# Kernel optimization log

Measured on AMD Instinct MI355X. Metric: run time of the kernel, lower is better.

## Reference

```python
import jax, jax.numpy as jnp
import numpy as np

B, T, E, D, V, L, A = 32, 800, 512, 1024, 5000, 149, 512
SOS, EOS = 1, 2


def setup_inputs() -> dict:
    key = jax.random.key(0)
    ks = jax.random.split(key, 20)
    s = 0.02
    inp = {
        'hpad': jax.random.normal(ks[0], (B, T, E), dtype=jnp.float32),
        'hlen': jax.random.randint(ks[1], (B,), T // 2, T + 1),
        'ys': jax.random.randint(ks[2], (B, L), 3, V),
        # embedding + output projection
        'embed': jax.random.normal(ks[3], (V, D), dtype=jnp.float32) * s,
        'W_out': jax.random.normal(ks[4], (V, D), dtype=jnp.float32) * s,
        'b_out': jnp.zeros((V,), dtype=jnp.float32),
        # additive attention params
        'W_enc': jax.random.normal(ks[5], (E, A), dtype=jnp.float32) * s,
        'W_dec': jax.random.normal(ks[6], (D, A), dtype=jnp.float32) * s,
        'v_att': jax.random.normal(ks[7], (A,), dtype=jnp.float32) * s,
        # LSTMCell layer 0: input = [ey; att_c] of size D+E
        'W_ih0': jax.random.normal(ks[8], (4 * D, D + E), dtype=jnp.float32) * s,
        'b_ih0': jnp.zeros((4 * D,), dtype=jnp.float32),
        'W_hh0': jax.random.normal(ks[9], (4 * D, D), dtype=jnp.float32) * s,
        'b_hh0': jnp.zeros((4 * D,), dtype=jnp.float32),
        # LSTMCell layer 1: input = z0 of size D
        'W_ih1': jax.random.normal(ks[10], (4 * D, D), dtype=jnp.float32) * s,
        'b_ih1': jnp.zeros((4 * D,), dtype=jnp.float32),
        'W_hh1': jax.random.normal(ks[11], (4 * D, D), dtype=jnp.float32) * s,
        'b_hh1': jnp.zeros((4 * D,), dtype=jnp.float32),
    }
    return inp


def _lstm_cell(x, h, c, W_ih, b_ih, W_hh, b_hh):
    # torch.nn.LSTMCell gate order: i, f, g, o
    g = x @ W_ih.T + b_ih + h @ W_hh.T + b_hh
    i, f, gg, o = jnp.split(g, 4, axis=-1)
    c2 = jax.nn.sigmoid(f) * c + jax.nn.sigmoid(i) * jnp.tanh(gg)
    h2 = jax.nn.sigmoid(o) * jnp.tanh(c2)
    return h2, c2


def reference(hpad, hlen, ys, embed, W_out, b_out, W_enc, W_dec, v_att,
              W_ih0, b_ih0, W_hh0, b_hh0, W_ih1, b_ih1, W_hh1, b_hh1):
    mask = jnp.arange(T)[None, :] < hlen[:, None]          # [B,T]
    hpad = hpad * mask[..., None]                          # mask_by_length
    ys_in = jnp.concatenate([jnp.full((B, 1), SOS, ys.dtype), ys], axis=1)   # [B,L+1]
    ys_out = jnp.concatenate([ys, jnp.full((B, 1), EOS, ys.dtype)], axis=1)  # [B,L+1]
    eys = embed[ys_in]                                     # [B,L+1,D]
    pe = jnp.einsum('bte,ea->bta', hpad, W_enc)            # precomputed enc proj

    def step(carry, ey):
        z0, c0, z1, c1 = carry
        # additive attention: e = v^T tanh(W_enc h + W_dec z0)
        e = jnp.einsum('bta,a->bt', jnp.tanh(pe + (z0 @ W_dec)[:, None, :]), v_att)
        e = jnp.where(mask, e, -1e30)
        w = jax.nn.softmax(e, axis=-1)                     # [B,T]
        att_c = jnp.einsum('bt,bte->be', w, hpad)          # [B,E]
        z0, c0 = _lstm_cell(jnp.concatenate([ey, att_c], axis=1), z0, c0,
                            W_ih0, b_ih0, W_hh0, b_hh0)
        z1, c1 = _lstm_cell(z0, z1, c1, W_ih1, b_ih1, W_hh1, b_hh1)
        logits = z1 @ W_out.T + b_out                      # [B,V]
        return (z0, c0, z1, c1), logits

    z = jnp.zeros((B, D), dtype=hpad.dtype)
    carry0 = (z, z, z, z)
    _, logits = jax.lax.scan(step, carry0, eys.transpose(1, 0, 2))  # [L+1,B,V]
    logits = logits.transpose(1, 0, 2)                     # [B,L+1,V]

    logp = jax.nn.log_softmax(logits, axis=-1)
    nll = -jnp.take_along_axis(logp, ys_out[..., None], axis=-1)[..., 0]
    # F.cross_entropy mean, then * (mean(len ys_in) - 1) = * L
    loss = nll.mean() * L
    acc = (jnp.argmax(logits, axis=-1) == ys_out).mean()
    return loss, acc
```

## Files before the change

kernel.cpp:

```cpp
#include <hip/hip_runtime.h>


typedef unsigned short u16;
typedef unsigned char u8;
typedef long long i64;
typedef unsigned long long u64;
typedef float f32x4 __attribute__((ext_vector_type(4)));
typedef float f32x2 __attribute__((ext_vector_type(2)));
typedef short s16x8 __attribute__((ext_vector_type(8)));

constexpr int cB = 32, cT = 800, cE = 512, cD = 1024, cV = 5000, cL = 149,
              cNS = 150, cA = 512;
constexpr int SOS = 1, EOS = 2;
constexpr int NBLK = 256;
constexpr float DS = 1.0f / 128.0f;

__device__ __forceinline__ float bf2f(u16 x){
  union { unsigned u; float f; } v; v.u = ((unsigned)x) << 16; return v.f;
}
__device__ __forceinline__ u16 f2bf(float f){
  union { float f; unsigned u; } v; v.f = f;
  unsigned r = v.u + 0x7FFFu + ((v.u >> 16) & 1u);
  return (u16)(r >> 16);
}
__device__ __forceinline__ float frcp(float x){ return __builtin_amdgcn_rcpf(x); }
__device__ __forceinline__ float fsigm(float x){ return frcp(1.f + __expf(-x)); }
__device__ __forceinline__ float ftanh(float x){
  float u = __expf(2.f * x);
  return 1.f - 2.f * frcp(u + 1.f);
}
__device__ __forceinline__ f32x4 MFMA(s16x8 a, s16x8 b, f32x4 c){
  return __builtin_amdgcn_mfma_f32_16x16x32_bf16(a, b, c, 0, 0, 0);
}
__device__ __forceinline__ f32x4 MFMA8(i64 a, i64 b, f32x4 c){
  return __builtin_amdgcn_mfma_f32_16x16x32_fp8_fp8(a, b, c, 0, 0, 0);
}
__device__ __forceinline__ s16x8 LD8(const u16* p){ return *(const s16x8*)p; }
__device__ __forceinline__ u8 f2fp8(float x){
  return (u8)(__builtin_amdgcn_cvt_pk_fp8_f32(x, x, 0, false) & 0xFF);
}
__device__ __forceinline__ unsigned pk4(float a, float b, float c, float d){
  unsigned w = (unsigned)__builtin_amdgcn_cvt_pk_fp8_f32(a, b, 0, false);
  w = (unsigned)__builtin_amdgcn_cvt_pk_fp8_f32(c, d, (int)w, true);
  return w;
}
__device__ __forceinline__ void unpack8(unsigned lo, unsigned hi, float* o){
  f32x2 a = __builtin_amdgcn_cvt_pk_f32_fp8((int)lo, false);
  f32x2 b = __builtin_amdgcn_cvt_pk_f32_fp8((int)lo, true);
  f32x2 c = __builtin_amdgcn_cvt_pk_f32_fp8((int)hi, false);
  f32x2 d = __builtin_amdgcn_cvt_pk_f32_fp8((int)hi, true);
  o[0]=a[0]; o[1]=a[1]; o[2]=b[0]; o[3]=b[1];
  o[4]=c[0]; o[5]=c[1]; o[6]=d[0]; o[7]=d[1];
}

__device__ __forceinline__ float ld_sc(const float* p){
  return __hip_atomic_load(p, __ATOMIC_RELAXED, __HIP_MEMORY_SCOPE_AGENT);
}
__device__ __forceinline__ void st_sc(float* p, float v){
  __hip_atomic_store(p, v, __ATOMIC_RELAXED, __HIP_MEMORY_SCOPE_AGENT);
}
__device__ __forceinline__ u64 ld_sc8(const void* p){
  return __hip_atomic_load((const u64*)p, __ATOMIC_RELAXED, __HIP_MEMORY_SCOPE_AGENT);
}
__device__ __forceinline__ void st_scb(u8* p, u8 v){
  __hip_atomic_store(p, v, __ATOMIC_RELAXED, __HIP_MEMORY_SCOPE_AGENT);
}

__global__ void k_init(int* bar, float* q, float* c0, float* c1, u8* z1f8,
                       float* att_acc, float* att_l){
  int i = blockIdx.x * blockDim.x + threadIdx.x, n = gridDim.x * blockDim.x;
  for (int k = i; k < 512; k += n) bar[k] = 0;
  for (int k = i; k < cB * cA; k += n) q[k] = 0.f;
  for (int k = i; k < 2 * cB * cD; k += n){ c0[k] = 0.f; c1[k] = 0.f; }
  for (int k = i; k < cB * cD / 4; k += n) ((unsigned*)z1f8)[k] = 0;
  for (int k = i; k < cB * cE; k += n) att_acc[k] = 0.f;
  for (int k = i; k < cB; k += n) att_l[k] = 0.f;
}

__global__ void k_cvt(const float* __restrict__ s, u16* __restrict__ d, int n4){
  int i = blockIdx.x * blockDim.x + threadIdx.x, st = gridDim.x * blockDim.x;
  for (int k = i; k < n4; k += st){
    float4 v = ((const float4*)s)[k];
    ushort4 o; o.x = f2bf(v.x); o.y = f2bf(v.y); o.z = f2bf(v.z); o.w = f2bf(v.w);
    ((ushort4*)d)[k] = o;
  }
}

__global__ void k_cvt8I(const float* __restrict__ s, u8* __restrict__ d, int n){
  int i = blockIdx.x * blockDim.x + threadIdx.x, st = gridDim.x * blockDim.x;
  for (int k = i; k < n; k += st){
    int row = k >> 6, grp = k & 63;
    const float4* p = (const float4*)(s + (size_t)row * 512 + grp * 8);
    float4 v0 = p[0], v1 = p[1];
    unsigned lo = pk4(v0.x, v0.y, v0.z, v0.w);
    unsigned hi = pk4(v1.x, v1.y, v1.z, v1.w);
    *(uint2*)(d + (size_t)row * 1024 + grp * 16 + 8) = make_uint2(lo, hi);
  }
}

__global__ void k_slice(const float* __restrict__ s, u16* __restrict__ d, int n,
                        int cshift, int srcld, int coff){
  int i = blockIdx.x * blockDim.x + threadIdx.x, st = gridDim.x * blockDim.x;
  int cmask = (1 << cshift) - 1;
  for (int k = i; k < n; k += st){
    int r = k >> cshift, c = k & cmask;
    d[k] = f2bf(s[(size_t)r * srcld + coff + c]);
  }
}

__global__ void k_transp(const float* __restrict__ s, u16* __restrict__ d, int n,
                         int rshift, int csrc){
  int i = blockIdx.x * blockDim.x + threadIdx.x, st = gridDim.x * blockDim.x;
  int mask = (1 << rshift) - 1;
  for (int k = i; k < n; k += st){
    int dd = k & mask, a = k >> rshift;
    d[k] = f2bf(s[(size_t)dd * csrc + a]);
  }
}

__global__ void k_bias(const float* a, const float* b, float* o, int n){
  int i = blockIdx.x * blockDim.x + threadIdx.x, st = gridDim.x * blockDim.x;
  for (int k = i; k < n; k += st) o[k] = a[k] + b[k];
}

__global__ void k_wf8perm(const float* __restrict__ s, u8* __restrict__ d,
                          int n4, int kshift, int srcld, int coff){
  int i = blockIdx.x * blockDim.x + threadIdx.x, st = gridDim.x * blockDim.x;
  int kmask = (1 << kshift) - 1;
  for (int k = i; k < n4; k += st){
    int flat = k * 4;
    int R = flat >> kshift, kk = flat & kmask;
    int j = R >> 5, jj = R & 31, g = jj >> 3, c = jj & 7;
    const float* p = s + (size_t)(g * 1024 + j * 8 + c) * srcld + coff + kk;
    ((unsigned*)d)[k] = pk4(p[0]*16.f, p[1]*16.f, p[2]*16.f, p[3]*16.f);
  }
}

__global__ void k_wf8(const float* __restrict__ s, u8* __restrict__ d, int n4){
  int i = blockIdx.x * blockDim.x + threadIdx.x, st = gridDim.x * blockDim.x;
  for (int k = i; k < n4; k += st){
    float4 v = ((const float4*)s)[k];
    ((unsigned*)d)[k] = pk4(v.x*16.f, v.y*16.f, v.z*16.f, v.w*16.f);
  }
}

__global__ void k_wf8t(const float* __restrict__ s, u8* __restrict__ d, int n4){
  int i = blockIdx.x * blockDim.x + threadIdx.x, st = gridDim.x * blockDim.x;
  for (int k = i; k < n4; k += st){
    int flat = k * 4;
    int a = flat >> 10, dd = flat & 1023;
    ((unsigned*)d)[k] = pk4(s[(size_t)(dd+0)*512 + a]*16.f,
                            s[(size_t)(dd+1)*512 + a]*16.f,
                            s[(size_t)(dd+2)*512 + a]*16.f,
                            s[(size_t)(dd+3)*512 + a]*16.f);
  }
}

__global__ void k_gather(const u16* __restrict__ embb, const int* __restrict__ ys,
                         u16* __restrict__ ey, int n16){
  int i = blockIdx.x * blockDim.x + threadIdx.x, st = gridDim.x * blockDim.x;
  for (int k = i; k < n16; k += st){
    int r = k >> 7, seg = k & 127;
    int s = r >> 5, b = r & 31;
    int tok = (s == 0) ? SOS : ys[b * cL + (s - 1)];
    ((uint4*)ey)[(size_t)r * 128 + seg] =
        ((const uint4*)embb)[(size_t)tok * 128 + seg];
  }
}

__global__ __launch_bounds__(512, 1) void k_pe2(const u16* __restrict__ A,
    const u16* __restrict__ Bw, u8* __restrict__ ph8){
  int tid = threadIdx.x, w = tid >> 6, l = tid & 63;
  int col = l & 15, kin = 8 * (l >> 4);
  int mw = w >> 2, nw = w & 3;
  int m0 = blockIdx.x * 128 + mw * 64;
  int n0 = nw * 128;
  f32x4 acc[4][8] = {};
  for (int kc = 0; kc < 16; ++kc){
    int k = kc * 32 + kin;
    s16x8 af[4], bf[8];
    #pragma unroll
    for (int i = 0; i < 4; ++i) af[i] = LD8(A + (size_t)(m0 + i*16 + col)*512 + k);
    #pragma unroll
    for (int j = 0; j < 8; ++j) bf[j] = LD8(Bw + (size_t)(n0 + j*16 + col)*512 + k);
    #pragma unroll
    for (int i = 0; i < 4; ++i)
      #pragma unroll
      for (int j = 0; j < 8; ++j) acc[i][j] = MFMA(af[i], bf[j], acc[i][j]);
  }
  int hi4 = (l >> 4) * 4;
  #pragma unroll
  for (int i = 0; i < 4; ++i)
    #pragma unroll
    for (int j = 0; j < 8; ++j){
      int a0 = n0 + j * 16 + col;
      size_t boff = ((size_t)(a0 >> 3) << 4) + (a0 & 7);
      #pragma unroll
      for (int r = 0; r < 4; ++r){
        int row = m0 + i * 16 + hi4 + r;
        ph8[(size_t)row * 1024 + boff] = f2fp8(acc[i][j][r]);
      }
    }
}

__global__ __launch_bounds__(512, 1) void k_ey2(const u16* __restrict__ ey,
    const u16* __restrict__ Wm, const float* __restrict__ bih0,
    const float* __restrict__ bhh0, u16* __restrict__ eyproj,
    float* __restrict__ g0buf){
  int tid = threadIdx.x, w = tid >> 6, l = tid & 63;
  int col = l & 15, kin = 8 * (l >> 4);
  int mw = w >> 2, nw = w & 3;
  int m0 = blockIdx.x * 128 + mw * 64;
  int n0 = blockIdx.y * 512 + nw * 128;
  f32x4 acc[4][8] = {};
  for (int kc = 0; kc < 32; ++kc){
    int k = kc * 32 + kin;
    s16x8 af[4], bf[8];
    #pragma unroll
    for (int i = 0; i < 4; ++i){
      int ar = m0 + i * 16 + col; ar = (ar < 4800) ? ar : 0;
      af[i] = LD8(ey + (size_t)ar * 1024 + k);
    }
    #pragma unroll
    for (int j = 0; j < 8; ++j) bf[j] = LD8(Wm + (size_t)(n0 + j*16 + col)*1024 + k);
    #pragma unroll
    for (int i = 0; i < 4; ++i)
      #pragma unroll
      for (int j = 0; j < 8; ++j) acc[i][j] = MFMA(af[i], bf[j], acc[i][j]);
  }
  int hi4 = (l >> 4) * 4;
  #pragma unroll
  for (int i = 0; i < 4; ++i)
    #pragma unroll
    for (int j = 0; j < 8; ++j){
      int jc = n0 + j * 16 + col;
      float bj = bih0[jc] + bhh0[jc];
      #pragma unroll
      for (int r = 0; r < 4; ++r){
        int row = m0 + i * 16 + hi4 + r;
        if (row < 4800){
          float val = acc[i][j][r] + bj;
          eyproj[(size_t)row * 4096 + jc] = f2bf(val);
          if (row < 32) g0buf[(size_t)row * 4096 + jc] = val;
        }
      }
    }
}

struct LoopArgs {
  const int* hlen;
  const u8* ph8;
  const u16* eyproj;
  const u8* Wapf8; const u8* Whh1f8; const u8* Wih1f8; const u8* Whh0f8;
  const u8* WdecTf8;
  const float* vatt; const float* bias01;
  float* q; float* att_acc; float* att_l;
  float* g0buf; float* hh1buf; u8* z0f8; u8* z1f8;
  float* c0; float* c1; u16* z1all;
  int* bar;
};

constexpr int SPZ = 1048;
constexpr int SPA = 536;

struct P1Lds { float red[8][512]; float ls[8]; };
struct GvLds { u8 x[32 * SPZ]; float acc[8][2][16][16]; };
union LoopLds { P1Lds p1; GvLds gv; };

__device__ __forceinline__ void gbar(int* bar, int blk, int target){
  __syncthreads();
  if (threadIdx.x == 0){
    asm volatile("s_waitcnt vmcnt(0)" ::: "memory");
    __hip_atomic_store(&bar[blk], target, __ATOMIC_RELAXED, __HIP_MEMORY_SCOPE_AGENT);
  }
  if (blk == NBLK - 1){
    if (threadIdx.x < NBLK){
      while (__hip_atomic_load(&bar[threadIdx.x], __ATOMIC_RELAXED,
                               __HIP_MEMORY_SCOPE_AGENT) < target)
        __builtin_amdgcn_s_sleep(1);
    }
    __syncthreads();
    if (threadIdx.x < 8)
      __hip_atomic_store(&bar[256 + threadIdx.x * 16], target, __ATOMIC_RELAXED,
                         __HIP_MEMORY_SCOPE_AGENT);
  }
  if (threadIdx.x == 0){
    int* rel = &bar[256 + (blk >> 5) * 16];
    while (__hip_atomic_load(rel, __ATOMIC_RELAXED,
                             __HIP_MEMORY_SCOPE_AGENT) < target)
      __builtin_amdgcn_s_sleep(1);
  }
  __syncthreads();
}

__device__ __forceinline__ void stage_att(LoopLds& L, const float* att_acc,
                                          const float* att_l, int tid){
  int r = tid >> 4, c0 = (tid & 15) * 32;
  float sc = 8.0f / ld_sc(att_l + r);
  const float* src = att_acc + r * 512 + c0;
  unsigned wd[8];
  #pragma unroll
  for (int i = 0; i < 8; ++i){
    union { u64 q; float f[2]; } a, b;
    a.q = ld_sc8(src + i * 4);
    b.q = ld_sc8(src + i * 4 + 2);
    wd[i] = pk4(a.f[0] * sc, a.f[1] * sc, b.f[0] * sc, b.f[1] * sc);
  }
  uint2* dst = (uint2*)&L.gv.x[r * SPA + c0];
  dst[0] = make_uint2(wd[0], wd[1]);
  dst[1] = make_uint2(wd[2], wd[3]);
  dst[2] = make_uint2(wd[4], wd[5]);
  dst[3] = make_uint2(wd[6], wd[7]);
}

__device__ __forceinline__ void stage_z(LoopLds& L, const u8* zf8, int tid){
  int r = tid >> 4, c0 = (tid & 15) * 64;
  const u8* src = zf8 + (size_t)r * 1024 + c0;
  u64 v[8];
  #pragma unroll
  for (int i = 0; i < 8; ++i) v[i] = ld_sc8(src + i * 8);
  u64* dst = (u64*)&L.gv.x[r * SPZ + c0];
  #pragma unroll
  for (int i = 0; i < 8; ++i) dst[i] = v[i];
}

template<int KH, int ITERS, int SP>
__device__ __forceinline__ void gemv_reg(const i64* wreg, LoopLds& L, int tid){
  const int w = tid >> 6, l = tid & 63;
  const int col = l & 15, kin = 8 * (l >> 4);
  const int kh = (KH == 4) ? (w & 3) : (w & 1);
  constexpr int KB = ITERS * 32;
  const u8* xr = &L.gv.x[col * SP + kh * KB + kin];
  f32x4 a0 = {0.f,0.f,0.f,0.f}, a1 = {0.f,0.f,0.f,0.f};
  #pragma unroll
  for (int kc = 0; kc < ITERS; ++kc){
    i64 x0 = *(const i64*)(xr + kc * 32);
    i64 x1 = *(const i64*)(xr + 16 * SP + kc * 32);
    a0 = MFMA8(x0, wreg[kc], a0);
    a1 = MFMA8(x1, wreg[kc], a1);
  }
  const int hi4 = (l >> 4) * 4;
  #pragma unroll
  for (int r = 0; r < 4; ++r){
    L.gv.acc[w][0][hi4 + r][col] = a0[r];
    L.gv.acc[w][1][hi4 + r][col] = a1[r];
  }
}

__global__ __launch_bounds__(512, 1) void k_loop(LoopArgs g_){
  __shared__ __align__(16) LoopLds L;
  __shared__ __align__(16) u8 ph8_lds[100 * 1024];
  const int blk = blockIdx.x, tid = threadIdx.x;
  const int w = tid >> 6, l = tid & 63;
  const int col = l & 15, kin = 8 * (l >> 4);
  const int b_att = blk >> 3, oct = blk & 7;
  const int hl = g_.hlen[b_att];
  const int t0 = oct * 100;
  const int t1 = (t0 + 100 < hl) ? t0 + 100 : hl;
  const int nrow = t1 - t0;
  float vv[8];
  #pragma unroll
  for (int i = 0; i < 8; ++i) vv[i] = g_.vatt[l * 8 + i];
  for (int idx = tid; idx < nrow * 64; idx += 512){
    int rr = idx >> 6, gg = idx & 63;
    *(uint4*)&ph8_lds[rr * 1024 + gg * 16] =
        *(const uint4*)(g_.ph8 + ((size_t)b_att * cT + t0 + rr) * 1024 + gg * 16);
  }
  i64 wB[8], wC[16];
  {
    const int nt4 = w >> 2, kh4 = w & 3;
    const int nt2 = w >> 1, kh2 = w & 1;
    if (blk < 128){
      const u8* wr = g_.Wapf8 + (size_t)blk * 32 * 512 +
                     (size_t)(nt4 * 16 + col) * 512 + kh4 * 128 + kin;
      #pragma unroll
      for (int kc = 0; kc < 4; ++kc) wB[kc] = *(const i64*)(wr + kc * 32);
      const u8* wr2 = g_.Wih1f8 + (size_t)blk * 32 * 1024 +
                      (size_t)(nt4 * 16 + col) * 1024 + kh4 * 256 + kin;
      #pragma unroll
      for (int kc = 0; kc < 8; ++kc) wC[kc] = *(const i64*)(wr2 + kc * 32);
    } else {
      const u8* wr = g_.Whh1f8 + (size_t)(blk - 128) * 32 * 1024 +
                     (size_t)(nt4 * 16 + col) * 1024 + kh4 * 256 + kin;
      #pragma unroll
      for (int kc = 0; kc < 8; ++kc) wB[kc] = *(const i64*)(wr + kc * 32);
      if (blk < 192){
        const u8* wr2 = g_.Whh0f8 + (size_t)(blk - 128) * 64 * 1024 +
                        (size_t)(nt2 * 16 + col) * 1024 + kh2 * 512 + kin;
        #pragma unroll
        for (int kc = 0; kc < 16; ++kc) wC[kc] = *(const i64*)(wr2 + kc * 32);
      } else if (blk < 208){
        const u8* wr2 = g_.WdecTf8 + (size_t)(blk - 192) * 32 * 1024 +
                        (size_t)(nt4 * 16 + col) * 1024 + kh4 * 256 + kin;
        #pragma unroll
        for (int kc = 0; kc < 8; ++kc) wC[kc] = *(const i64*)(wr2 + kc * 32);
      }
    }
  }
  __syncthreads();
  int target = 0;
  for (int s = 0; s < cNS; ++s){
    const int p = s & 1;
    if (nrow > 0){
      float qv[8];
      const float* qb = g_.q + b_att * cA + l * 8;
      #pragma unroll
      for (int i = 0; i < 8; ++i) qv[i] = ld_sc(qb + i);
      float acc8[8] = {0.f,0.f,0.f,0.f,0.f,0.f,0.f,0.f};
      float lsum = 0.f;
      for (int t = t0 + w; t < t1; t += 8){
        uint4 v = *(const uint4*)&ph8_lds[(t - t0) * 1024 + l * 16];
        float x[8]; unpack8(v.x, v.y, x);
        float e_ = 0.f;
        #pragma unroll
        for (int i = 0; i < 8; ++i) e_ += vv[i] * ftanh(x[i] + qv[i]);
        #pragma unroll
        for (int m = 1; m < 64; m <<= 1) e_ += __shfl_xor(e_, m, 64);
        float wt = __expf(e_);
        lsum += wt;
        float h[8]; unpack8(v.z, v.w, h);
        #pragma unroll
        for (int i = 0; i < 8; ++i) acc8[i] = fmaf(wt, h[i], acc8[i]);
      }
      *(f32x4*)&L.p1.red[w][l * 8]     = *(f32x4*)&acc8[0];
      *(f32x4*)&L.p1.red[w][l * 8 + 4] = *(f32x4*)&acc8[4];
      if (l == 0) L.p1.ls[w] = lsum;
      __syncthreads();
      float vsum = 0.f;
      #pragma unroll
      for (int ww = 0; ww < 8; ++ww) vsum += L.p1.red[ww][tid];
      atomicAdd(&g_.att_acc[b_att * cE + tid], vsum);
      if (tid == 0){
        float ls = 0.f;
        #pragma unroll
        for (int i = 0; i < 8; ++i) ls += L.p1.ls[i];
        atomicAdd(&g_.att_l[b_att], ls);
      }
    }
    gbar(g_.bar, blk, ++target);
    if (blk < 128){
      stage_att(L, g_.att_acc, g_.att_l, tid);
      __syncthreads();
      gemv_reg<4, 4, SPA>(wB, L, tid);
      __syncthreads();
      if (tid < 256){
        int b = tid >> 3, dc = tid & 7, d = blk * 8 + dc;
        int mt = b >> 4, rr = b & 15;
        float gate[4];
        #pragma unroll
        for (int g = 0; g < 4; ++g){
          int jj = g * 8 + dc;
          float v = 0.f;
          #pragma unroll
          for (int kh = 0; kh < 4; ++kh)
            v += L.gv.acc[(jj >> 4) * 4 + kh][mt][rr][jj & 15];
          gate[g] = v * DS +
                    ld_sc(&g_.g0buf[(size_t)p * cB * 4096 + b * 4096 + g * 1024 + d]);
        }
        float c = fsigm(gate[1]) * g_.c0[(size_t)p * cB * cD + b * cD + d] +
                  fsigm(gate[0]) * ftanh(gate[2]);
        float z = fsigm(gate[3]) * ftanh(c);
        g_.c0[(size_t)(p ^ 1) * cB * cD + b * cD + d] = c;
        st_scb(&g_.z0f8[b * cD + d], f2fp8(z * 8.f));
      }
    } else {
      stage_z(L, g_.z1f8, tid);
      __syncthreads();
      gemv_reg<4, 8, SPZ>(wB, L, tid);
      __syncthreads();
      const int jb = (blk - 128) * 32;
      #pragma unroll
      for (int it = 0; it < 2; ++it){
        int idx = it * 512 + tid;
        int b = idx >> 5, jj = idx & 31;
        int mt = b >> 4, rr = b & 15;
        float v = 0.f;
        #pragma unroll
        for (int kh = 0; kh < 4; ++kh)
          v += L.gv.acc[(jj >> 4) * 4 + kh][mt][rr][jj & 15];
        st_sc(&g_.hh1buf[b * 4096 + jb + jj], v * DS + g_.bias01[jb + jj]);
      }
    }
    gbar(g_.bar, blk, ++target);
    if (blk < 128){
      stage_z(L, g_.z0f8, tid);
      __syncthreads();
      gemv_reg<4, 8, SPZ>(wC, L, tid);
      __syncthreads();
      if (tid < 256){
        int b = tid >> 3, dc = tid & 7, d = blk * 8 + dc;
        int mt = b >> 4, rr = b & 15;
        float gate[4];
        #pragma unroll
        for (int g = 0; g < 4; ++g){
          int jj = g * 8 + dc;
          float v = 0.f;
          #pragma unroll
          for (int kh = 0; kh < 4; ++kh)
            v += L.gv.acc[(jj >> 4) * 4 + kh][mt][rr][jj & 15];
          gate[g] = v * DS + ld_sc(&g_.hh1buf[b * 4096 + g * 1024 + d]);
        }
        float c = fsigm(gate[1]) * g_.c1[(size_t)p * cB * cD + b * cD + d] +
                  fsigm(gate[0]) * ftanh(gate[2]);
        float z = fsigm(gate[3]) * ftanh(c);
        g_.c1[(size_t)(p ^ 1) * cB * cD + b * cD + d] = c;
        g_.z1all[((size_t)s + 1) * cB * cD + b * cD + d] = f2bf(z);
        st_scb(&g_.z1f8[b * cD + d], f2fp8(z * 8.f));
      }
    } else if (blk < 192){
      stage_z(L, g_.z0f8, tid);
      __syncthreads();
      gemv_reg<2, 16, SPZ>(wC, L, tid);
      __syncthreads();
      if (s < cNS - 1){
        const int jb = (blk - 128) * 64;
        #pragma unroll
        for (int it = 0; it < 4; ++it){
          int idx = it * 512 + tid;
          int b = idx >> 6, jj = idx & 63;
          int mt = b >> 4, rr = b & 15;
          float v = 0.f;
          #pragma unroll
          for (int kh = 0; kh < 2; ++kh)
            v += L.gv.acc[(jj >> 4) * 2 + kh][mt][rr][jj & 15];
          st_sc(&g_.g0buf[(size_t)(p ^ 1) * cB * 4096 + b * 4096 + jb + jj],
                v * DS + bf2f(g_.eyproj[(((size_t)s + 1) * cB + b) * 4096 + jb + jj]));
        }
      }
    } else if (blk < 208){
      stage_z(L, g_.z0f8, tid);
      __syncthreads();
      gemv_reg<4, 8, SPZ>(wC, L, tid);
      __syncthreads();
      if (s < cNS - 1){
        const int jb = (blk - 192) * 32;
        #pragma unroll
        for (int it = 0; it < 2; ++it){
          int idx = it * 512 + tid;
          int b = idx >> 5, jj = idx & 31;
          int mt = b >> 4, rr = b & 15;
          float v = 0.f;
          #pragma unroll
          for (int kh = 0; kh < 4; ++kh)
            v += L.gv.acc[(jj >> 4) * 4 + kh][mt][rr][jj & 15];
          st_sc(&g_.q[b * cA + jb + jj], v * DS);
        }
      }
    } else if (blk == 208){
      for (int i = tid; i < cB * cE; i += 512) st_sc(&g_.att_acc[i], 0.f);
      if (tid < 32) st_sc(&g_.att_l[tid], 0.f);
    }
    gbar(g_.bar, blk, ++target);
  }
}

__global__ __launch_bounds__(256) void k_ce1(const u16* __restrict__ z1all,
    const u16* __restrict__ Woutb, const float* __restrict__ bout,
    const int* __restrict__ ys, float* __restrict__ pmax, float* __restrict__ psum,
    int* __restrict__ pai, float* __restrict__ tgtl){
  int blk = blockIdx.x;
  int sc = blk / 40, vc = blk % 40;
  int tid = threadIdx.x, w = tid >> 6, l = tid & 63;
  int kin = 8 * (l >> 4), col = l & 15;
  int v0 = vc * 128 + w * 32;
  int vA = v0 + col, vB = v0 + 16 + col;
  float boA = (vA < cV) ? bout[vA] : 0.f;
  float boB = (vB < cV) ? bout[vB] : 0.f;
  const u16* wrA = Woutb + (size_t)((vA < cV) ? vA : cV - 1) * cD;
  const u16* wrB = Woutb + (size_t)((vB < cV) ? vB : cV - 1) * cD;
  __shared__ int tgt_sh[32];
  __shared__ float rsm[4][32], rss[4][32];
  __shared__ int rsi[4][32];
  for (int si = 0; si < 5; ++si){
    int s = sc * 5 + si;
    if (tid < 32) tgt_sh[tid] = (s < cL) ? ys[tid * cL + s] : EOS;
    __syncthreads();
    const u16* z1s = z1all + ((size_t)s + 1) * cB * cD;
    f32x4 aA0 = {0.f,0.f,0.f,0.f}, aA1 = {0.f,0.f,0.f,0.f};
    f32x4 aB0 = {0.f,0.f,0.f,0.f}, aB1 = {0.f,0.f,0.f,0.f};
    for (int kc = 0; kc < 32; ++kc){
      int k = kc * 32 + kin;
      s16x8 x0 = LD8(z1s + (size_t)col * cD + k);
      s16x8 x1 = LD8(z1s + (size_t)(16 + col) * cD + k);
      s16x8 bA = LD8(wrA + k);
      s16x8 bB = LD8(wrB + k);
      aA0 = MFMA(x0, bA, aA0); aA1 = MFMA(x1, bA, aA1);
      aB0 = MFMA(x0, bB, aB0); aB1 = MFMA(x1, bB, aB1);
    }
    #pragma unroll
    for (int mt = 0; mt < 2; ++mt)
    #pragma unroll
    for (int reg = 0; reg < 4; ++reg){
      int row = mt * 16 + (l >> 4) * 4 + reg;
      float va = (mt ? aA1[reg] : aA0[reg]) + boA; if (vA >= cV) va = -1e30f;
      float vb = (mt ? aB1[reg] : aB0[reg]) + boB; if (vB >= cV) vb = -1e30f;
      int tg = tgt_sh[row];
      if (vA == tg) tgtl[(size_t)s * cB + row] = va;
      if (vB == tg) tgtl[(size_t)s * cB + row] = vb;
      float mx = fmaxf(va, vb);
      int ix = (va >= vb) ? vA : vB;
      #pragma unroll
      for (int m = 1; m < 16; m <<= 1){
        float om = __shfl_xor(mx, m, 64);
        int oi = __shfl_xor(ix, m, 64);
        if (om > mx || (om == mx && oi < ix)){ mx = om; ix = oi; }
// ... 49 lines not shown
    nll += __shfl_xor(nll, m, 64); cor += __shfl_xor(cor, m, 64);
  }
  if (tid == 0){ cestep[s * 2] = nll; cestep[s * 2 + 1] = cor; }
}

__global__ __launch_bounds__(256) void k_ce3(const float* __restrict__ cestep,
                                             float* __restrict__ out){
  int tid = threadIdx.x;
  float nll = 0.f, cor = 0.f;
  for (int s = tid; s < cNS; s += 256){ nll += cestep[s * 2]; cor += cestep[s * 2 + 1]; }
  __shared__ float sn[4], sc_[4];
  int w = tid >> 6, l = tid & 63;
  #pragma unroll
  for (int m = 1; m < 64; m <<= 1){
    nll += __shfl_xor(nll, m, 64); cor += __shfl_xor(cor, m, 64);
  }
  if (l == 0){ sn[w] = nll; sc_[w] = cor; }
  __syncthreads();
  if (tid == 0){
    float a = sn[0] + sn[1] + sn[2] + sn[3];
    float b = sc_[0] + sc_[1] + sc_[2] + sc_[3];
    out[0] = a / (float)(cB * cNS) * (float)cL;
    out[1] = b / (float)(cB * cNS);
  }
}

extern "C" void kernel_launch(void* const* d_in, const int* in_sizes, int n_in,
                              void* d_out, int out_size, void* d_ws, size_t ws_size,
                              hipStream_t stream){
  const float* hpad = (const float*)d_in[0];
  const int*   hlen = (const int*)d_in[1];
  const int*   ys   = (const int*)d_in[2];
  const float* embed= (const float*)d_in[3];
  const float* Wout = (const float*)d_in[4];
  const float* bout = (const float*)d_in[5];
  const float* Wenc = (const float*)d_in[6];
  const float* Wdec = (const float*)d_in[7];
  const float* vatt = (const float*)d_in[8];
  const float* Wih0 = (const float*)d_in[9];
  const float* bih0 = (const float*)d_in[10];
  const float* Whh0 = (const float*)d_in[11];
  const float* bhh0 = (const float*)d_in[12];
  const float* Wih1 = (const float*)d_in[13];
  const float* bih1 = (const float*)d_in[14];
  const float* Whh1 = (const float*)d_in[15];
  const float* bhh1 = (const float*)d_in[16];
  (void)in_sizes; (void)n_in; (void)out_size; (void)ws_size;

  char* base = (char*)d_ws;
  size_t off = 0;
  auto alloc = [&](size_t bytes) -> void* {
    void* r = base + off; off += (bytes + 255) & ~(size_t)255; return r;
  };
  int*   bar     = (int*)  alloc(512 * sizeof(int));
  u16*   hpadM   = (u16*)  alloc((size_t)cB * cT * cE * 2);
  u8*    ph8     = (u8*)   alloc((size_t)cB * cT * 1024);
  u16*   embb    = (u16*)  alloc((size_t)cV * cD * 2);
  u16*   ey      = (u16*)  alloc((size_t)cNS * cB * cD * 2);
  u16*   eyproj  = (u16*)  alloc((size_t)cNS * cB * 4096 * 2);
  u16*   z1all   = (u16*)  alloc((size_t)(cNS + 1) * cB * cD * 2);
  u16*   WencT   = (u16*)  alloc((size_t)cA * cE * 2);
  u16*   Wih0m   = (u16*)  alloc((size_t)4096 * cD * 2);
  u16*   Woutb   = (u16*)  alloc((size_t)cV * cD * 2);
  u8*    Wapf8   = (u8*)   alloc((size_t)4096 * 512);
  u8*    Wih1f8  = (u8*)   alloc((size_t)4096 * 1024);
  u8*    Whh1f8  = (u8*)   alloc((size_t)4096 * 1024);
  u8*    Whh0f8  = (u8*)   alloc((size_t)4096 * 1024);
  u8*    WdecTf8 = (u8*)   alloc((size_t)512 * 1024);
  float* bias01  = (float*)alloc(4096 * 4);
  float* qbuf    = (float*)alloc((size_t)cB * cA * 4);
  float* att_acc = (float*)alloc((size_t)cB * cE * 4);
  float* att_l   = (float*)alloc((size_t)cB * 4);
  float* g0buf   = (float*)alloc((size_t)2 * cB * 4096 * 4);
  float* hh1buf  = (float*)alloc((size_t)cB * 4096 * 4);
  u8*    z0f8    = (u8*)   alloc((size_t)cB * cD);
  u8*    z1f8    = (u8*)   alloc((size_t)cB * cD);
  float* c0      = (float*)alloc((size_t)2 * cB * cD * 4);
  float* c1      = (float*)alloc((size_t)2 * cB * cD * 4);
  float* pmax    = (float*)alloc((size_t)cNS * cB * 40 * 4);
  float* psum    = (float*)alloc((size_t)cNS * cB * 40 * 4);
  int*   pai     = (int*)  alloc((size_t)cNS * cB * 40 * 4);
  float* tgtl    = (float*)alloc((size_t)cNS * cB * 4);
  float* cestep  = (float*)alloc((size_t)cNS * 2 * 4);

  k_init<<<64, 256, 0, stream>>>(bar, qbuf, c0, c1, z1f8, att_acc, att_l);
  k_cvt<<<2048, 256, 0, stream>>>(hpad, hpadM, cB * cT * cE / 4);
  k_cvt8I<<<1024, 256, 0, stream>>>(hpad, ph8, cB * cT * 64);
  k_cvt<<<2048, 256, 0, stream>>>(embed, embb, cV * cD / 4);
  k_cvt<<<2048, 256, 0, stream>>>(Wout, Woutb, cV * cD / 4);
  k_slice<<<1024, 256, 0, stream>>>(Wih0, Wih0m, 4096 * cD, 10, 1536, 0);
  k_transp<<<256, 256, 0, stream>>>(Wenc, WencT, cA * cE, 9, cA);
  k_bias<<<16, 256, 0, stream>>>(bih1, bhh1, bias01, 4096);
  k_wf8perm<<<512, 256, 0, stream>>>(Wih0, Wapf8, 4096 * 512 / 4, 9, 1536, 1024);
  k_wf8perm<<<1024, 256, 0, stream>>>(Wih1, Wih1f8, 4096 * 1024 / 4, 10, 1024, 0);
  k_wf8<<<1024, 256, 0, stream>>>(Whh1, Whh1f8, 4096 * 1024 / 4);
  k_wf8<<<1024, 256, 0, stream>>>(Whh0, Whh0f8, 4096 * 1024 / 4);
  k_wf8t<<<128, 256, 0, stream>>>(Wdec, WdecTf8, 512 * 1024 / 4);
  k_gather<<<1200, 256, 0, stream>>>(embb, ys, ey, cNS * cB * 128);
  k_pe2<<<200, 512, 0, stream>>>(hpadM, WencT, ph8);
  k_ey2<<<dim3(38, 8), 512, 0, stream>>>(ey, Wih0m, bih0, bhh0, eyproj, g0buf);

  LoopArgs la;
  la.hlen = hlen; la.ph8 = ph8; la.eyproj = eyproj;
  la.Wapf8 = Wapf8; la.Whh1f8 = Whh1f8; la.Wih1f8 = Wih1f8;
  la.Whh0f8 = Whh0f8; la.WdecTf8 = WdecTf8;
  la.vatt = vatt; la.bias01 = bias01;
  la.q = qbuf; la.att_acc = att_acc; la.att_l = att_l;
  la.g0buf = g0buf; la.hh1buf = hh1buf; la.z0f8 = z0f8; la.z1f8 = z1f8;
  la.c0 = c0; la.c1 = c1; la.z1all = z1all; la.bar = bar;
  k_loop<<<NBLK, 512, 0, stream>>>(la);

  k_ce1<<<1200, 256, 0, stream>>>(z1all, Woutb, bout, ys, pmax, psum, pai, tgtl);
  k_ce2<<<cNS, 64, 0, stream>>>(pmax, psum, pai, tgtl, ys, cestep);
  k_ce3<<<1, 256, 0, stream>>>(cestep, (float*)d_out);
}
```

Baseline: 4.657 ms.

## Replace grid-wide barriers with per-stage dataflow counters in persistent decoder loop

```diff
diff --git a/kernel.cpp b/kernel.cpp
--- a/kernel.cpp
+++ b/kernel.cpp
@@ -3,6 +3,7 @@
 
 typedef unsigned short u16;
 typedef unsigned char u8;
+typedef unsigned int u32;
 typedef long long i64;
 typedef unsigned long long u64;
 typedef float f32x4 __attribute__((ext_vector_type(4)));
@@ -15,12 +16,15 @@
 constexpr int NBLK = 256;
 constexpr float DS = 1.0f / 128.0f;
 
+constexpr int ACNT = 0, Z0CNT = 128, HH1CNT = 256, Z1CNT = 384, G0CNT = 512,
+              QCNT = 640, SCNT = 768 , ZDONE = 1024 ;
+
 __device__ __forceinline__ float bf2f(u16 x){
-  union { unsigned u; float f; } v; v.u = ((unsigned)x) << 16; return v.f;
+  union { u32 u; float f; } v; v.u = ((u32)x) << 16; return v.f;
 }
 __device__ __forceinline__ u16 f2bf(float f){
-  union { float f; unsigned u; } v; v.f = f;
-  unsigned r = v.u + 0x7FFFu + ((v.u >> 16) & 1u);
+  union { float f; u32 u; } v; v.f = f;
+  u32 r = v.u + 0x7FFFu + ((v.u >> 16) & 1u);
   return (u16)(r >> 16);
 }
 __device__ __forceinline__ float frcp(float x){ return __builtin_amdgcn_rcpf(x); }
@@ -39,12 +43,12 @@
 __device__ __forceinline__ u8 f2fp8(float x){
   return (u8)(__builtin_amdgcn_cvt_pk_fp8_f32(x, x, 0, false) & 0xFF);
 }
-__device__ __forceinline__ unsigned pk4(float a, float b, float c, float d){
-  unsigned w = (unsigned)__builtin_amdgcn_cvt_pk_fp8_f32(a, b, 0, false);
-  w = (unsigned)__builtin_amdgcn_cvt_pk_fp8_f32(c, d, (int)w, true);
+__device__ __forceinline__ u32 pk4(float a, float b, float c, float d){
+  u32 w = (u32)__builtin_amdgcn_cvt_pk_fp8_f32(a, b, 0, false);
+  w = (u32)__builtin_amdgcn_cvt_pk_fp8_f32(c, d, (int)w, true);
   return w;
 }
-__device__ __forceinline__ void unpack8(unsigned lo, unsigned hi, float* o){
+__device__ __forceinline__ void unpack8(u32 lo, u32 hi, float* o){
   f32x2 a = __builtin_amdgcn_cvt_pk_f32_fp8((int)lo, false);
   f32x2 b = __builtin_amdgcn_cvt_pk_f32_fp8((int)lo, true);
   f32x2 c = __builtin_amdgcn_cvt_pk_f32_fp8((int)hi, false);
@@ -62,19 +66,40 @@
 __device__ __forceinline__ u64 ld_sc8(const void* p){
   return __hip_atomic_load((const u64*)p, __ATOMIC_RELAXED, __HIP_MEMORY_SCOPE_AGENT);
 }
+__device__ __forceinline__ u32 ld_su(const u32* p){
+  return __hip_atomic_load(p, __ATOMIC_RELAXED, __HIP_MEMORY_SCOPE_AGENT);
+}
+__device__ __forceinline__ void st_su(u32* p, u32 v){
+  __hip_atomic_store(p, v, __ATOMIC_RELAXED, __HIP_MEMORY_SCOPE_AGENT);
+}
 __device__ __forceinline__ void st_scb(u8* p, u8 v){
   __hip_atomic_store(p, v, __ATOMIC_RELAXED, __HIP_MEMORY_SCOPE_AGENT);
 }
 
-__global__ void k_init(int* bar, float* q, float* c0, float* c1, u8* z1f8,
+__device__ __forceinline__ void gate8(const u32* c, u32 target){
+  for(;;){
+    u32 s = 0;
+    #pragma unroll
+    for (int i = 0; i < 8; ++i) s += ld_su(c + i * 16);
+    if (s >= target) break;
+    __builtin_amdgcn_s_sleep(1);
+  }
+}
+__device__ __forceinline__ void inc8(u32* c, int blk){
+  asm volatile("s_waitcnt vmcnt(0)" ::: "memory");
+  __hip_atomic_fetch_add(c + (blk & 7) * 16, 1u, __ATOMIC_RELAXED,
+                         __HIP_MEMORY_SCOPE_AGENT);
+}
+
+__global__ void k_init(u32* ctl, float* q, float* c0, float* c1, u8* z1f8,
                        float* att_acc, float* att_l){
   int i = blockIdx.x * blockDim.x + threadIdx.x, n = gridDim.x * blockDim.x;
-  for (int k = i; k < 512; k += n) bar[k] = 0;
+  for (int k = i; k < 1152; k += n) ctl[k] = 0;
   for (int k = i; k < cB * cA; k += n) q[k] = 0.f;
   for (int k = i; k < 2 * cB * cD; k += n){ c0[k] = 0.f; c1[k] = 0.f; }
-  for (int k = i; k < cB * cD / 4; k += n) ((unsigned*)z1f8)[k] = 0;
-  for (int k = i; k < cB * cE; k += n) att_acc[k] = 0.f;
-  for (int k = i; k < cB; k += n) att_l[k] = 0.f;
+  for (int k = i; k < cB * cD / 4; k += n) ((u32*)z1f8)[k] = 0;
+  for (int k = i; k < 2 * cB * cE; k += n) att_acc[k] = 0.f;
+  for (int k = i; k < 2 * cB; k += n) att_l[k] = 0.f;
 }
 
 __global__ void k_cvt(const float* __restrict__ s, u16* __restrict__ d, int n4){
@@ -92,8 +117,8 @@
     int row = k >> 6, grp = k & 63;
     const float4* p = (const float4*)(s + (size_t)row * 512 + grp * 8);
     float4 v0 = p[0], v1 = p[1];
-    unsigned lo = pk4(v0.x, v0.y, v0.z, v0.w);
-    unsigned hi = pk4(v1.x, v1.y, v1.z, v1.w);
+    u32 lo = pk4(v0.x, v0.y, v0.z, v0.w);
+    u32 hi = pk4(v1.x, v1.y, v1.z, v1.w);
     *(uint2*)(d + (size_t)row * 1024 + grp * 16 + 8) = make_uint2(lo, hi);
   }
 }
@@ -132,7 +157,7 @@
     int R = flat >> kshift, kk = flat & kmask;
     int j = R >> 5, jj = R & 31, g = jj >> 3, c = jj & 7;
     const float* p = s + (size_t)(g * 1024 + j * 8 + c) * srcld + coff + kk;
-    ((unsigned*)d)[k] = pk4(p[0]*16.f, p[1]*16.f, p[2]*16.f, p[3]*16.f);
+    ((u32*)d)[k] = pk4(p[0]*16.f, p[1]*16.f, p[2]*16.f, p[3]*16.f);
   }
 }
 
@@ -140,7 +165,7 @@
   int i = blockIdx.x * blockDim.x + threadIdx.x, st = gridDim.x * blockDim.x;
   for (int k = i; k < n4; k += st){
     float4 v = ((const float4*)s)[k];
-    ((unsigned*)d)[k] = pk4(v.x*16.f, v.y*16.f, v.z*16.f, v.w*16.f);
+    ((u32*)d)[k] = pk4(v.x*16.f, v.y*16.f, v.z*16.f, v.w*16.f);
   }
 }
 
@@ -149,10 +174,10 @@
   for (int k = i; k < n4; k += st){
     int flat = k * 4;
     int a = flat >> 10, dd = flat & 1023;
-    ((unsigned*)d)[k] = pk4(s[(size_t)(dd+0)*512 + a]*16.f,
-                            s[(size_t)(dd+1)*512 + a]*16.f,
-                            s[(size_t)(dd+2)*512 + a]*16.f,
-                            s[(size_t)(dd+3)*512 + a]*16.f);
+    ((u32*)d)[k] = pk4(s[(size_t)(dd+0)*512 + a]*16.f,
+                       s[(size_t)(dd+1)*512 + a]*16.f,
+                       s[(size_t)(dd+2)*512 + a]*16.f,
+                       s[(size_t)(dd+3)*512 + a]*16.f);
   }
 }
 
@@ -257,87 +282,73 @@
   float* q; float* att_acc; float* att_l;
   float* g0buf; float* hh1buf; u8* z0f8; u8* z1f8;
   float* c0; float* c1; u16* z1all;
-  int* bar;
+  u32* ctl;
 };
 
-constexpr int SPZ = 1048;
-constexpr int SPA = 536;
-
 struct P1Lds { float red[8][512]; float ls[8]; };
-struct GvLds { u8 x[32 * SPZ]; float acc[8][2][16][16]; };
+struct GvLds { float acc[8][2][16][17]; };
 union LoopLds { P1Lds p1; GvLds gv; };
 
-__device__ __forceinline__ void gbar(int* bar, int blk, int target){
-  __syncthreads();
-  if (threadIdx.x == 0){
-    asm volatile("s_waitcnt vmcnt(0)" ::: "memory");
-    __hip_atomic_store(&bar[blk], target, __ATOMIC_RELAXED, __HIP_MEMORY_SCOPE_AGENT);
-  }
-  if (blk == NBLK - 1){
-    if (threadIdx.x < NBLK){
-      while (__hip_atomic_load(&bar[threadIdx.x], __ATOMIC_RELAXED,
-                               __HIP_MEMORY_SCOPE_AGENT) < target)
-        __builtin_amdgcn_s_sleep(1);
-    }
-    __syncthreads();
-    if (threadIdx.x < 8)
-      __hip_atomic_store(&bar[256 + threadIdx.x * 16], target, __ATOMIC_RELAXED,
-                         __HIP_MEMORY_SCOPE_AGENT);
-  }
-  if (threadIdx.x == 0){
-    int* rel = &bar[256 + (blk >> 5) * 16];
-    while (__hip_atomic_load(rel, __ATOMIC_RELAXED,
-                             __HIP_MEMORY_SCOPE_AGENT) < target)
-      __builtin_amdgcn_s_sleep(1);
-  }
-  __syncthreads();
-}
-
-__device__ __forceinline__ void stage_att(LoopLds& L, const float* att_acc,
-                                          const float* att_l, int tid){
-  int r = tid >> 4, c0 = (tid & 15) * 32;
-  float sc = 8.0f / ld_sc(att_l + r);
-  const float* src = att_acc + r * 512 + c0;
-  unsigned wd[8];
-  #pragma unroll
-  for (int i = 0; i < 8; ++i){
-    union { u64 q; float f[2]; } a, b;
-    a.q = ld_sc8(src + i * 4);
-    b.q = ld_sc8(src + i * 4 + 2);
-    wd[i] = pk4(a.f[0] * sc, a.f[1] * sc, b.f[0] * sc, b.f[1] * sc);
-  }
-  uint2* dst = (uint2*)&L.gv.x[r * SPA + c0];
-  dst[0] = make_uint2(wd[0], wd[1]);
-  dst[1] = make_uint2(wd[2], wd[3]);
-  dst[2] = make_uint2(wd[4], wd[5]);
-  dst[3] = make_uint2(wd[6], wd[7]);
-}
-
-__device__ __forceinline__ void stage_z(LoopLds& L, const u8* zf8, int tid){
-  int r = tid >> 4, c0 = (tid & 15) * 64;
-  const u8* src = zf8 + (size_t)r * 1024 + c0;
-  u64 v[8];
-  #pragma unroll
-  for (int i = 0; i < 8; ++i) v[i] = ld_sc8(src + i * 8);
-  u64* dst = (u64*)&L.gv.x[r * SPZ + c0];
-  #pragma unroll
-  for (int i = 0; i < 8; ++i) dst[i] = v[i];
-}
-
-template<int KH, int ITERS, int SP>
-__device__ __forceinline__ void gemv_reg(const i64* wreg, LoopLds& L, int tid){
+template<int KH, int ITERS>
+__device__ __forceinline__ void gemv_dirz(const i64* wreg, const u8* zg,
+                                          LoopLds& L, int tid){
   const int w = tid >> 6, l = tid & 63;
   const int col = l & 15, kin = 8 * (l >> 4);
   const int kh = (KH == 4) ? (w & 3) : (w & 1);
   constexpr int KB = ITERS * 32;
-  const u8* xr = &L.gv.x[col * SP + kh * KB + kin];
+  const u8* xr = zg + (size_t)col * 1024 + kh * KB + kin;
+  i64 x0[ITERS], x1[ITERS];
+  #pragma unroll
+  for (int kc = 0; kc < ITERS; ++kc){
+    x0[kc] = (i64)ld_sc8(xr + kc * 32);
+    x1[kc] = (i64)ld_sc8(xr + 16 * 1024 + kc * 32);
+  }
   f32x4 a0 = {0.f,0.f,0.f,0.f}, a1 = {0.f,0.f,0.f,0.f};
   #pragma unroll
   for (int kc = 0; kc < ITERS; ++kc){
-    i64 x0 = *(const i64*)(xr + kc * 32);
-    i64 x1 = *(const i64*)(xr + 16 * SP + kc * 32);
-    a0 = MFMA8(x0, wreg[kc], a0);
-    a1 = MFMA8(x1, wreg[kc], a1);
+    a0 = MFMA8(x0[kc], wreg[kc], a0);
+    a1 = MFMA8(x1[kc], wreg[kc], a1);
+  }
+  const int hi4 = (l >> 4) * 4;
+  #pragma unroll
+  for (int r = 0; r < 4; ++r){
+    L.gv.acc[w][0][hi4 + r][col] = a0[r];
+    L.gv.acc[w][1][hi4 + r][col] = a1[r];
+  }
+}
+
+__device__ __forceinline__ void gemv_att(const i64* wreg, const float* aacc,
+                                         const float* al, LoopLds& L, int tid){
+  const int w = tid >> 6, l = tid & 63;
+  const int col = l & 15, kin = 8 * (l >> 4);
+  const int kh = w & 3;
+  const float* ar0 = aacc + (size_t)col * 512 + kh * 128 + kin;
+  const float* ar1 = aacc + (size_t)(col + 16) * 512 + kh * 128 + kin;
+  float s0 = 8.f * frcp(ld_sc(al + col));
+  float s1 = 8.f * frcp(ld_sc(al + col + 16));
+  u64 v0[16], v1[16];
+  #pragma unroll
+  for (int kc = 0; kc < 4; ++kc){
+    #pragma unroll
+    for (int j = 0; j < 4; ++j){
+      v0[kc*4+j] = ld_sc8(ar0 + kc * 32 + j * 2);
+      v1[kc*4+j] = ld_sc8(ar1 + kc * 32 + j * 2);
+    }
+  }
+  f32x4 a0 = {0.f,0.f,0.f,0.f}, a1 = {0.f,0.f,0.f,0.f};
+  #pragma unroll
+  for (int kc = 0; kc < 4; ++kc){
+    union { u64 q; u32 d[2]; } t0, t1;
+    #pragma unroll
+    for (int h = 0; h < 2; ++h){
+      union { u64 q; float f[2]; } aa, bb;
+      aa.q = v0[kc*4 + h*2]; bb.q = v0[kc*4 + h*2 + 1];
+      t0.d[h] = pk4(aa.f[0]*s0, aa.f[1]*s0, bb.f[0]*s0, bb.f[1]*s0);
+      aa.q = v1[kc*4 + h*2]; bb.q = v1[kc*4 + h*2 + 1];
+      t1.d[h] = pk4(aa.f[0]*s1, aa.f[1]*s1, bb.f[0]*s1, bb.f[1]*s1);
+    }
+    a0 = MFMA8((i64)t0.q, wreg[kc], a0);
+    a1 = MFMA8((i64)t1.q, wreg[kc], a1);
   }
   const int hi4 = (l >> 4) * 4;
   #pragma unroll
@@ -358,6 +369,7 @@
   const int t0 = oct * 100;
   const int t1 = (t0 + 100 < hl) ? t0 + 100 : hl;
   const int nrow = t1 - t0;
+  u32* ctl = g_.ctl;
   float vv[8];
   #pragma unroll
   for (int i = 0; i < 8; ++i) vv[i] = g_.vatt[l * 8 + i];
@@ -398,9 +410,17 @@
     }
   }
   __syncthreads();
-  int target = 0;
+
   for (int s = 0; s < cNS; ++s){
     const int p = s & 1;
+    if (tid == 0){
+      gate8(ctl + QCNT, 16u * (u32)s);
+      if (nrow > 0){
+        u32 need = (u32)(s >> 1);
+        while (ld_su(&ctl[ZDONE + p * 16]) < need) __builtin_amdgcn_s_sleep(2);
+      }
+    }
+    __syncthreads();
     if (nrow > 0){
       float qv[8];
       const float* qb = g_.q + b_att * cA + l * 8;
@@ -429,23 +449,28 @@
       float vsum = 0.f;
       #pragma unroll
       for (int ww = 0; ww < 8; ++ww) vsum += L.p1.red[ww][tid];
-      atomicAdd(&g_.att_acc[b_att * cE + tid], vsum);
+      atomicAdd(&g_.att_acc[((size_t)p * cB + b_att) * cE + tid], vsum);
       if (tid == 0){
         float ls = 0.f;
         #pragma unroll
         for (int i = 0; i < 8; ++i) ls += L.p1.ls[i];
-        atomicAdd(&g_.att_l[b_att], ls);
-      }
-    }
-    gbar(g_.bar, blk, ++target);
+        atomicAdd(&g_.att_l[p * cB + b_att], ls);
+      }
+    }
+    __syncthreads();
+    if (tid == 0) inc8(ctl + ACNT, blk);
     if (blk < 128){
-      stage_att(L, g_.att_acc, g_.att_l, tid);
-      __syncthreads();
-      gemv_reg<4, 4, SPA>(wB, L, tid);
-      __syncthreads();
+      if (tid == 0){
+        gate8(ctl + ACNT, 256u * (u32)(s + 1));
+        gate8(ctl + G0CNT, 64u * (u32)s);
+      }
+      __syncthreads();
+      gemv_att(wB, g_.att_acc + (size_t)p * cB * cE, g_.att_l + p * cB, L, tid);
+      __syncthreads();
+      if (tid == 0) inc8(ctl + SCNT + p * 128, blk);
       if (tid < 256){
-        int b = tid >> 3, dc = tid & 7, d = blk * 8 + dc;
-        int mt = b >> 4, rr = b & 15;
+        int bb = tid >> 3, dc = tid & 7, d = blk * 8 + dc;
+        int mt = bb >> 4, rr = bb & 15;
         float gate[4];
         #pragma unroll
         for (int g = 0; g < 4; ++g){
@@ -455,41 +480,49 @@
           for (int kh = 0; kh < 4; ++kh)
             v += L.gv.acc[(jj >> 4) * 4 + kh][mt][rr][jj & 15];
           gate[g] = v * DS +
-                    ld_sc(&g_.g0buf[(size_t)p * cB * 4096 + b * 4096 + g * 1024 + d]);
+                    ld_sc(&g_.g0buf[(size_t)p * cB * 4096 + bb * 4096 + g * 1024 + d]);
         }
-        float c = fsigm(gate[1]) * g_.c0[(size_t)p * cB * cD + b * cD + d] +
+        float c = fsigm(gate[1]) * g_.c0[(size_t)p * cB * cD + bb * cD + d] +
                   fsigm(gate[0]) * ftanh(gate[2]);
         float z = fsigm(gate[3]) * ftanh(c);
-        g_.c0[(size_t)(p ^ 1) * cB * cD + b * cD + d] = c;
-        st_scb(&g_.z0f8[b * cD + d], f2fp8(z * 8.f));
-      }
+        g_.c0[(size_t)(p ^ 1) * cB * cD + bb * cD + d] = c;
+        st_scb(&g_.z0f8[bb * cD + d], f2fp8(z * 8.f));
+      }
+      __syncthreads();
+      if (tid == 0) inc8(ctl + Z0CNT, blk);
     } else {
-      stage_z(L, g_.z1f8, tid);
-      __syncthreads();
-      gemv_reg<4, 8, SPZ>(wB, L, tid);
-      __syncthreads();
-      const int jb = (blk - 128) * 32;
-      #pragma unroll
-      for (int it = 0; it < 2; ++it){
-        int idx = it * 512 + tid;
-        int b = idx >> 5, jj = idx & 31;
-        int mt = b >> 4, rr = b & 15;
-        float v = 0.f;
-        #pragma unroll
-        for (int kh = 0; kh < 4; ++kh)
-          v += L.gv.acc[(jj >> 4) * 4 + kh][mt][rr][jj & 15];
-        st_sc(&g_.hh1buf[b * 4096 + jb + jj], v * DS + g_.bias01[jb + jj]);
-      }
-    }
-    gbar(g_.bar, blk, ++target);
+      if (tid == 0) gate8(ctl + Z1CNT, 128u * (u32)s);
+      __syncthreads();
+      gemv_dirz<4, 8>(wB, g_.z1f8, L, tid);
+      __syncthreads();
+      {
+        const int jb = (blk - 128) * 32;
+        int bb = tid >> 4, j2 = (tid & 15) * 2;
+        int mt = bb >> 4, rr = bb & 15;
+        #pragma unroll
+        for (int k = 0; k < 2; ++k){
+          int jj = j2 + k;
+          float v = 0.f;
+          #pragma unroll
+          for (int kh = 0; kh < 4; ++kh)
+            v += L.gv.acc[(jj >> 4) * 4 + kh][mt][rr][jj & 15];
+          st_sc(&g_.hh1buf[bb * 4096 + jb + jj], v * DS + g_.bias01[jb + jj]);
+        }
+      }
+      __syncthreads();
+      if (tid == 0) inc8(ctl + HH1CNT, blk);
+    }
     if (blk < 128){
-      stage_z(L, g_.z0f8, tid);
-      __syncthreads();
-      gemv_reg<4, 8, SPZ>(wC, L, tid);
+      if (tid == 0){
+        gate8(ctl + Z0CNT, 128u * (u32)(s + 1));
+        gate8(ctl + HH1CNT, 128u * (u32)(s + 1));
+      }
+      __syncthreads();
+      gemv_dirz<4, 8>(wC, g_.z0f8, L, tid);
       __syncthreads();
       if (tid < 256){
-        int b = tid >> 3, dc = tid & 7, d = blk * 8 + dc;
-        int mt = b >> 4, rr = b & 15;
+        int bb = tid >> 3, dc = tid & 7, d = blk * 8 + dc;
+        int mt = bb >> 4, rr = bb & 15;
         float gate[4];
         #pragma unroll
         for (int g = 0; g < 4; ++g){
@@ -498,59 +531,76 @@
           #pragma unroll
           for (int kh = 0; kh < 4; ++kh)
             v += L.gv.acc[(jj >> 4) * 4 + kh][mt][rr][jj & 15];
-          gate[g] = v * DS + ld_sc(&g_.hh1buf[b * 4096 + g * 1024 + d]);
+          gate[g] = v * DS + ld_sc(&g_.hh1buf[bb * 4096 + g * 1024 + d]);
         }
-        float c = fsigm(gate[1]) * g_.c1[(size_t)p * cB * cD + b * cD + d] +
+        float c = fsigm(gate[1]) * g_.c1[(size_t)p * cB * cD + bb * cD + d] +
                   fsigm(gate[0]) * ftanh(gate[2]);
         float z = fsigm(gate[3]) * ftanh(c);
-        g_.c1[(size_t)(p ^ 1) * cB * cD + b * cD + d] = c;
-        g_.z1all[((size_t)s + 1) * cB * cD + b * cD + d] = f2bf(z);
-        st_scb(&g_.z1f8[b * cD + d], f2fp8(z * 8.f));
-      }
+        g_.c1[(size_t)(p ^ 1) * cB * cD + bb * cD + d] = c;
+        g_.z1all[((size_t)s + 1) * cB * cD + bb * cD + d] = f2bf(z);
+        st_scb(&g_.z1f8[bb * cD + d], f2fp8(z * 8.f));
+      }
+      __syncthreads();
+      if (tid == 0) inc8(ctl + Z1CNT, blk);
     } else if (blk < 192){
-      stage_z(L, g_.z0f8, tid);
-      __syncthreads();
-      gemv_reg<2, 16, SPZ>(wC, L, tid);
+      if (tid == 0) gate8(ctl + Z0CNT, 128u * (u32)(s + 1));
+      __syncthreads();
+      gemv_dirz<2, 16>(wC, g_.z0f8, L, tid);
       __syncthreads();
       if (s < cNS - 1){
         const int jb = (blk - 128) * 64;
-        #pragma unroll
-        for (int it = 0; it < 4; ++it){
-          int idx = it * 512 + tid;
-          int b = idx >> 6, jj = idx & 63;
-          int mt = b >> 4, rr = b & 15;
+        int bb = tid >> 4, j4 = (tid & 15) * 4;
+        int mt = bb >> 4, rr = bb & 15;
+        const u16* eyr = g_.eyproj + (((size_t)(s + 1) * cB + bb) * 4096) + jb + j4;
+        #pragma unroll
+        for (int k = 0; k < 4; ++k){
+          int jj = j4 + k;
           float v = 0.f;
           #pragma unroll
           for (int kh = 0; kh < 2; ++kh)
             v += L.gv.acc[(jj >> 4) * 2 + kh][mt][rr][jj & 15];
-          st_sc(&g_.g0buf[(size_t)(p ^ 1) * cB * 4096 + b * 4096 + jb + jj],
-                v * DS + bf2f(g_.eyproj[(((size_t)s + 1) * cB + b) * 4096 + jb + jj]));
+          st_sc(&g_.g0buf[(size_t)(p ^ 1) * cB * 4096 + bb * 4096 + jb + jj],
+                v * DS + bf2f(eyr[k]));
         }
       }
+      __syncthreads();
+      if (tid == 0) inc8(ctl + G0CNT, blk);
     } else if (blk < 208){
-      stage_z(L, g_.z0f8, tid);
-      __syncthreads();
-      gemv_reg<4, 8, SPZ>(wC, L, tid);
+      if (tid == 0) gate8(ctl + Z0CNT, 128u * (u32)(s + 1));
+      __syncthreads();
+      gemv_dirz<4, 8>(wC, g_.z0f8, L, tid);
       __syncthreads();
       if (s < cNS - 1){
         const int jb = (blk - 192) * 32;
-        #pragma unroll
-        for (int it = 0; it < 2; ++it){
-          int idx = it * 512 + tid;
-          int b = idx >> 5, jj = idx & 31;
-          int mt = b >> 4, rr = b & 15;
+        int bb = tid >> 4, j2 = (tid & 15) * 2;
+        int mt = bb >> 4, rr = bb & 15;
+        #pragma unroll
+        for (int k = 0; k < 2; ++k){
+          int jj = j2 + k;
           float v = 0.f;
           #pragma unroll
           for (int kh = 0; kh < 4; ++kh)
             v += L.gv.acc[(jj >> 4) * 4 + kh][mt][rr][jj & 15];
-          st_sc(&g_.q[b * cA + jb + jj], v * DS);
+          st_sc(&g_.q[bb * cA + jb + jj], v * DS);
         }
       }
+      __syncthreads();
+      if (tid == 0) inc8(ctl + QCNT, blk);
     } else if (blk == 208){
-      for (int i = tid; i < cB * cE; i += 512) st_sc(&g_.att_acc[i], 0.f);
-      if (tid < 32) st_sc(&g_.att_l[tid], 0.f);
-    }
-    gbar(g_.bar, blk, ++target);
+      if (tid == 0)
+        gate8(ctl + SCNT + p * 128, 128u * ((u32)(s >> 1) + 1u));
+      __syncthreads();
+      {
+        float* aa = g_.att_acc + (size_t)p * cB * cE;
+        for (int i = tid; i < cB * cE; i += 512) st_sc(&aa[i], 0.f);
+        if (tid < cB) st_sc(&g_.att_l[p * cB + tid], 0.f);
+      }
+      __syncthreads();
+      if (tid == 0){
+        asm volatile("s_waitcnt vmcnt(0)" ::: "memory");
+        st_su(&ctl[ZDONE + p * 16], (u32)(s >> 1) + 1u);
+      }
+    }
   }
 }
 
@@ -706,7 +756,7 @@
   auto alloc = [&](size_t bytes) -> void* {
     void* r = base + off; off += (bytes + 255) & ~(size_t)255; return r;
   };
-  int*   bar     = (int*)  alloc(512 * sizeof(int));
+  u32*   ctl     = (u32*)  alloc(1152 * 4);
   u16*   hpadM   = (u16*)  alloc((size_t)cB * cT * cE * 2);
   u8*    ph8     = (u8*)   alloc((size_t)cB * cT * 1024);
   u16*   embb    = (u16*)  alloc((size_t)cV * cD * 2);
@@ -723,8 +773,8 @@
   u8*    WdecTf8 = (u8*)   alloc((size_t)512 * 1024);
   float* bias01  = (float*)alloc(4096 * 4);
   float* qbuf    = (float*)alloc((size_t)cB * cA * 4);
-  float* att_acc = (float*)alloc((size_t)cB * cE * 4);
-  float* att_l   = (float*)alloc((size_t)cB * 4);
+  float* att_acc = (float*)alloc((size_t)2 * cB * cE * 4);
+  float* att_l   = (float*)alloc((size_t)2 * cB * 4);
   float* g0buf   = (float*)alloc((size_t)2 * cB * 4096 * 4);
   float* hh1buf  = (float*)alloc((size_t)cB * 4096 * 4);
   u8*    z0f8    = (u8*)   alloc((size_t)cB * cD);
@@ -737,7 +787,7 @@
   float* tgtl    = (float*)alloc((size_t)cNS * cB * 4);
   float* cestep  = (float*)alloc((size_t)cNS * 2 * 4);
 
-  k_init<<<64, 256, 0, stream>>>(bar, qbuf, c0, c1, z1f8, att_acc, att_l);
+  k_init<<<64, 256, 0, stream>>>(ctl, qbuf, c0, c1, z1f8, att_acc, att_l);
   k_cvt<<<2048, 256, 0, stream>>>(hpad, hpadM, cB * cT * cE / 4);
   k_cvt8I<<<1024, 256, 0, stream>>>(hpad, ph8, cB * cT * 64);
   k_cvt<<<2048, 256, 0, stream>>>(embed, embb, cV * cD / 4);
@@ -761,7 +811,7 @@
   la.vatt = vatt; la.bias01 = bias01;
   la.q = qbuf; la.att_acc = att_acc; la.att_l = att_l;
   la.g0buf = g0buf; la.hh1buf = hh1buf; la.z0f8 = z0f8; la.z1f8 = z1f8;
-  la.c0 = c0; la.c1 = c1; la.z1all = z1all; la.bar = bar;
+  la.c0 = c0; la.c1 = c1; la.z1all = z1all; la.ctl = ctl;
   k_loop<<<NBLK, 512, 0, stream>>>(la);
 
   k_ce1<<<1200, 256, 0, stream>>>(z1all, Woutb, bout, ys, pmax, psum, pai, tgtl);
```

New measurement: 5.722 ms. 1.23x slower.
